# Kernel tuning notes

Hardware: AMD Instinct MI355X
Metric: run time of the kernel (lower is better)

The kernel has to match this reference:

```python
import jax, jax.numpy as jnp
import numpy as np

D_MODEL = 768
N_HEADS = 12
D_HEAD = D_MODEL // N_HEADS
B, T = 2, 4096


def setup_inputs() -> dict:
    key = jax.random.key(0)
    ks = jax.random.split(key, 9)
    s = 1.0 / np.sqrt(D_MODEL)
    x = jax.random.normal(ks[0], (B, T, D_MODEL), dtype=jnp.float32)
    Wq = jax.random.uniform(ks[1], (D_MODEL, D_MODEL), jnp.float32, -s, s)
    Wk = jax.random.uniform(ks[2], (D_MODEL, D_MODEL), jnp.float32, -s, s)
    Wv = jax.random.uniform(ks[3], (D_MODEL, D_MODEL), jnp.float32, -s, s)
    Wo = jax.random.uniform(ks[4], (D_MODEL, D_MODEL), jnp.float32, -s, s)
    bq = jax.random.uniform(ks[5], (D_MODEL,), jnp.float32, -s, s)
    bk = jax.random.uniform(ks[6], (D_MODEL,), jnp.float32, -s, s)
    bv = jax.random.uniform(ks[7], (D_MODEL,), jnp.float32, -s, s)
    bo = jax.random.uniform(ks[8], (D_MODEL,), jnp.float32, -s, s)
    return {"x": x, "Wq": Wq, "bq": bq, "Wk": Wk, "bk": bk,
            "Wv": Wv, "bv": bv, "Wo": Wo, "bo": bo}


def _split_heads(t):
    # [B, T, D] -> [B, H, T, d_head]
    Bc, Tc, _ = t.shape
    return t.reshape(Bc, Tc, N_HEADS, D_HEAD).transpose(0, 2, 1, 3)


def reference(x, Wq, bq, Wk, bk, Wv, bv, Wo, bo):
    scale = D_HEAD ** -0.5
    Q = _split_heads(x @ Wq.T + bq)
    K = _split_heads(x @ Wk.T + bk)
    V = _split_heads(x @ Wv.T + bv)
    scores = jnp.einsum('bhqd,bhkd->bhqk', Q, K) * scale  # [B,H,T,T]
    attn = jax.nn.softmax(scores, axis=-1)
    out = jnp.einsum('bhqk,bhkd->bhqd', attn, V)  # [B,H,T,d_head]
    out = out.transpose(0, 2, 1, 3).reshape(x.shape[0], x.shape[1], D_MODEL)
    return out @ Wo.T + bo
```

## Files before the change

kernel.cpp:

```cpp
#include <hip/hip_runtime.h>
#include <hip/hip_bf16.h>

#define DM 768
#define NH 12
#define TB 2
#define TT 4096
#define MM (TB*TT)
#define NQKV (3*DM)
#define NW (DM*DM)
#define NX (MM*DM)
#define CEQ 0.18033688f

typedef unsigned short u16;
typedef short s16x8 __attribute__((ext_vector_type(8)));
typedef unsigned short u16x8 __attribute__((ext_vector_type(8)));
typedef float f32x4 __attribute__((ext_vector_type(4)));
typedef float f32x16 __attribute__((ext_vector_type(16)));
typedef unsigned u32x4 __attribute__((ext_vector_type(4)));

#if __has_builtin(__builtin_amdgcn_exp2f)
#define EXP2 __builtin_amdgcn_exp2f
#else
#define EXP2 exp2f
#endif

__device__ __forceinline__ u16 f2bf(float f) {
  unsigned u = __builtin_bit_cast(unsigned, f);
  unsigned r = (u + 0x7FFFu + ((u >> 16) & 1u)) >> 16;
  return (u16)r;
}

__device__ __forceinline__ unsigned cvtpk(float lo, float hi) {
  unsigned r;
  asm("v_cvt_pk_bf16_f32 %0, %1, %2" : "=v"(r) : "v"(lo), "v"(hi));
  return r;
}

__device__ __forceinline__ void gload16(const void* g, void* l) {
  __builtin_amdgcn_global_load_lds(
      (const __attribute__((address_space(1))) void*)g,
      (__attribute__((address_space(3))) void*)l, 16, 0, 0);
}

__device__ __forceinline__ void plswap(unsigned a, unsigned b, unsigned& r0, unsigned& r1) {
#if __has_builtin(__builtin_amdgcn_permlane32_swap)
  auto rr = __builtin_amdgcn_permlane32_swap(a, b, false, false);
  unsigned tmp[2];
  __builtin_memcpy(tmp, &rr, 8);
  r0 = tmp[0]; r1 = tmp[1];
#else
  int hi_ = (threadIdx.x >> 5) & 1;
  unsigned bx = (unsigned)__shfl_xor((int)b, 32, 64);
  unsigned ax = (unsigned)__shfl_xor((int)a, 32, 64);
  r0 = hi_ ? bx : a;
  r1 = hi_ ? b : ax;
#endif
}

__device__ __forceinline__ float xhalf_sum(float v) {
  unsigned a = __builtin_bit_cast(unsigned, v), r0, r1;
  plswap(a, a, r0, r1);
  return __builtin_bit_cast(float, r0) + __builtin_bit_cast(float, r1);
}

__device__ __forceinline__ void repack2(const f32x16& sv, s16x8& fa, s16x8& fb) {
  {
    unsigned cA0 = cvtpk(sv[0], sv[1]),  cA1 = cvtpk(sv[2], sv[3]);
    unsigned cB0 = cvtpk(sv[4], sv[5]),  cB1 = cvtpk(sv[6], sv[7]);
    unsigned w0, w1, w2, w3;
    plswap(cA0, cB0, w0, w2);
    plswap(cA1, cB1, w1, w3);
    u32x4 w = {w0, w1, w2, w3};
    fa = __builtin_bit_cast(s16x8, w);
  }
  {
    unsigned cA0 = cvtpk(sv[8], sv[9]),   cA1 = cvtpk(sv[10], sv[11]);
    unsigned cB0 = cvtpk(sv[12], sv[13]), cB1 = cvtpk(sv[14], sv[15]);
    unsigned w0, w1, w2, w3;
    plswap(cA0, cB0, w0, w2);
    plswap(cA1, cB1, w1, w3);
    u32x4 w = {w0, w1, w2, w3};
    fb = __builtin_bit_cast(s16x8, w);
  }
}

__device__ __forceinline__ float tree16(const f32x16& u) {
  float a0 = u[0] + u[8],  a1 = u[1] + u[9],  a2 = u[2] + u[10], a3 = u[3] + u[11];
  float a4 = u[4] + u[12], a5 = u[5] + u[13], a6 = u[6] + u[14], a7 = u[7] + u[15];
  a0 += a4; a1 += a5; a2 += a6; a3 += a7;
  a0 += a2; a1 += a3;
  return a0 + a1;
}

__global__ __launch_bounds__(256) void cast_prep(
    const float* __restrict__ x, const float* __restrict__ wq,
    const float* __restrict__ wk, const float* __restrict__ wv,
    const float* __restrict__ wo, const float* __restrict__ bq,
    const float* __restrict__ bk, const float* __restrict__ bv,
    u16* __restrict__ xb, u16* __restrict__ wqkvb, u16* __restrict__ wob,
    float* __restrict__ bqkv) {
  int g = blockIdx.x * 256 + threadIdx.x;
  int e = g * 4;
  const float* src;
  u16* dst;
  if (e < NX) { src = x + e; dst = xb + e; }
  else {
    int e2 = e - NX;
    if (e2 < 3*NW) {
      const float* w = (e2 < NW) ? wq : (e2 < 2*NW ? wk : wv);
      int base = (e2 < NW) ? 0 : (e2 < 2*NW ? NW : 2*NW);
      src = w + (e2 - base); dst = wqkvb + e2;
    } else { int e3 = e2 - 3*NW; src = wo + e3; dst = wob + e3; }
  }
  float4 v = *(const float4*)src;
  ushort4 p;
  p.x = f2bf(v.x); p.y = f2bf(v.y); p.z = f2bf(v.z); p.w = f2bf(v.w);
  *(ushort4*)dst = p;
  if (blockIdx.x == 0) {
    for (int i = threadIdx.x; i < NQKV; i += 256)
      bqkv[i] = (i < DM) ? bq[i] : (i < 2*DM ? bk[i-DM] : bv[i-2*DM]);
  }
}

__global__ __launch_bounds__(256, 3) void gemm_qkv(
    const u16* __restrict__ A, const u16* __restrict__ W,
    const float* __restrict__ bias,
    u16* __restrict__ qb, u16* __restrict__ kb, u16* __restrict__ vt) {
  __shared__ __align__(16) u16 As[2][128*32], Bs[2][128*32];
  const int tid = threadIdx.x, lane = tid & 63, wave = tid >> 6;
  const int rg = lane & 15, cg = lane >> 4;
  int lin = blockIdx.y * 18 + blockIdx.x;
  int swz = (lin & 7) * 144 + (lin >> 3);
  const int m0 = (swz / 18) * 128, n0 = (swz % 18) * 128;
  const int wm = (wave >> 1) * 64, wn = (wave & 1) * 64;
  f32x4 acc[4][4];
#pragma unroll
  for (int i = 0; i < 4; i++)
#pragma unroll
    for (int j = 0; j < 4; j++) acc[i][j] = (f32x4){0.f,0.f,0.f,0.f};

  const u16* ga = A + (size_t)(m0 + (tid >> 2)) * DM + (tid & 3) * 8;
  const u16* gb = W + (size_t)(n0 + (tid >> 2)) * DM + (tid & 3) * 8;
  auto stage = [&](int kt, int buf) {
    int ko = kt * 32;
    char* la = (char*)&As[buf][0] + wave * 1024;
    char* lb = (char*)&Bs[buf][0] + wave * 1024;
    gload16(ga + ko,                    la);
    gload16(ga + (size_t)64*DM + ko,    la + 4096);
    gload16(gb + ko,                    lb);
    gload16(gb + (size_t)64*DM + ko,    lb + 4096);
  };

  stage(0, 0);
  __syncthreads();
  const int NT = DM / 32;
  int cur = 0;
  for (int kt = 0; kt < NT; ++kt) {
    if (kt + 1 < NT) stage(kt + 1, cur ^ 1);
    s16x8 af[4], bfv[4];
#pragma unroll
    for (int i = 0; i < 4; i++) af[i]  = *(const s16x8*)&As[cur][(wm + i*16 + rg)*32 + cg*8];
#pragma unroll
    for (int i = 0; i < 4; i++) bfv[i] = *(const s16x8*)&Bs[cur][(wn + i*16 + rg)*32 + cg*8];
    __builtin_amdgcn_s_setprio(1);
#pragma unroll
    for (int mi = 0; mi < 4; mi++)
#pragma unroll
      for (int ni = 0; ni < 4; ni++)
        acc[mi][ni] = __builtin_amdgcn_mfma_f32_16x16x32_bf16(af[mi], bfv[ni], acc[mi][ni], 0, 0, 0);
    __builtin_amdgcn_s_setprio(0);
    __syncthreads();
    cur ^= 1;
  }

#pragma unroll
  for (int ni = 0; ni < 4; ni++) {
    int o = n0 + wn + ni*16 + rg;
    float bia = bias[o];
    int mat = o / DM, d = o % DM;
    int head = d >> 6, dh = d & 63;
    if (mat == 2) {
#pragma unroll
      for (int mi = 0; mi < 4; mi++) {
        int m = m0 + wm + mi*16 + cg*4;
        int b = m >> 12, t = m & 4095;
        ushort4 pv;
        pv.x = f2bf(acc[mi][ni][0] + bia);
        pv.y = f2bf(acc[mi][ni][1] + bia);
        pv.z = f2bf(acc[mi][ni][2] + bia);
        pv.w = f2bf(acc[mi][ni][3] + bia);
        *(ushort4*)&vt[((size_t)((b*NH + head)*64 + dh))*TT + t] = pv;
      }
    } else {
      u16* outp = mat ? kb : qb;
      float sc = mat ? 1.0f : CEQ;
#pragma unroll
      for (int mi = 0; mi < 4; mi++) {
#pragma unroll
        for (int r = 0; r < 4; r++) {
          int m = m0 + wm + mi*16 + cg*4 + r;
          int b = m >> 12, t = m & 4095;
          outp[((size_t)((b*NH + head)*TT + t))*64 + dh] = f2bf((acc[mi][ni][r] + bia) * sc);
        }
      }
    }
  }
}

__global__ __launch_bounds__(128, 2) void attn5(
    const u16* __restrict__ qg, const u16* __restrict__ kg,
    const u16* __restrict__ vtg, u16* __restrict__ h) {
  __shared__ __align__(16) char smem[32768];
  const int tid = threadIdx.x, lane = tid & 63, wave = tid >> 6;
  const int ql = lane & 31, hi = lane >> 5;
  int lin = blockIdx.y * 32 + blockIdx.x;
  int swz = (lin & 7) * 96 + (lin >> 3);
  int qt = swz & 31, bh = swz >> 5;
  const int b = bh / NH, head = bh % NH;
  const size_t hb = (size_t)bh * TT * 64;

  const int qrowA = qt * 128 + wave * 64 + ql;
  const u16* qpA = qg + hb + (size_t)qrowA * 64 + hi * 8;
  s16x8 qfA[4], qfB[4];
#pragma unroll
  for (int ds = 0; ds < 4; ++ds) {
    qfA[ds] = *(const s16x8*)(qpA + ds * 16);
    qfB[ds] = *(const s16x8*)(qpA + 32*64 + ds * 16);
  }

  const int lr = lane >> 3;
  const int lc = ((lane & 7) ^ lr) * 16;
  const char* kSrc = (const char*)(kg + hb) + lr * 128 + lc;
  const char* vSrc = (const char*)(vtg + hb) + (size_t)lr * 8192 + lc;
  auto stage = [&](int kt, int buf) {
    char* lk = smem + buf * 16384 + wave * 4096;
    char* lv = lk + 8192;
    const char* gk = kSrc + (size_t)kt * 8192 + wave * 4096;
    const char* gv = vSrc + (size_t)kt * 128 + (size_t)wave * 262144;
#pragma unroll
    for (int i = 0; i < 4; ++i) {
      gload16(gk + i*1024,  lk + i*1024);
      gload16(gv + i*65536, lv + i*1024);
    }
  };

  f32x16 oA0 = {}, oA1 = {}, oB0 = {}, oB1 = {};
  float LA = 0.f, LB = 0.f;
  const int swb = (ql & 7) << 4;

  stage(0, 0);
  __syncthreads();

  const int NKT = TT / 64;
  int cur = 0;
  for (int kt = 0; kt < NKT; ++kt) {
    if (kt + 1 < NKT) stage(kt + 1, cur ^ 1);
    const char* Kt = smem + cur * 16384;
    const char* Vt = Kt + 8192;
#pragma unroll
    for (int c = 0; c < 2; ++c) {
      const char* bkc = Kt + (c*32 + ql) * 128;
      s16x8 kf[4];
#pragma unroll
      for (int ds = 0; ds < 4; ++ds)
        kf[ds] = *(const s16x8*)(bkc + ((ds*32 + hi*16) ^ swb));
      f32x16 sA = {}, sB = {};
      __builtin_amdgcn_s_setprio(1);
#pragma unroll
      for (int ds = 0; ds < 4; ++ds) {
        sA = __builtin_amdgcn_mfma_f32_32x32x16_bf16(kf[ds], qfA[ds], sA, 0, 0, 0);
        sB = __builtin_amdgcn_mfma_f32_32x32x16_bf16(kf[ds], qfB[ds], sB, 0, 0, 0);
      }
      __builtin_amdgcn_s_setprio(0);
      const char* bvc = Vt + ql * 128;
      s16x8 vf[2][2];
#pragma unroll
      for (int hh = 0; hh < 2; ++hh)
#pragma unroll
        for (int kc = 0; kc < 2; ++kc)
          vf[hh][kc] = *(const s16x8*)(bvc + hh*4096 + ((c*64 + kc*32 + hi*16) ^ swb));
#pragma unroll
      for (int i = 0; i < 16; ++i) sA[i] = EXP2(sA[i]);
#pragma unroll
      for (int i = 0; i < 16; ++i) sB[i] = EXP2(sB[i]);
      LA += tree16(sA);
      LB += tree16(sB);
      s16x8 pfA[2], pfB[2];
      repack2(sA, pfA[0], pfA[1]);
      repack2(sB, pfB[0], pfB[1]);
      __builtin_amdgcn_s_setprio(1);
#pragma unroll
      for (int kc = 0; kc < 2; ++kc) {
        oA0 = __builtin_amdgcn_mfma_f32_32x32x16_bf16(vf[0][kc], pfA[kc], oA0, 0, 0, 0);
        oB0 = __builtin_amdgcn_mfma_f32_32x32x16_bf16(vf[0][kc], pfB[kc], oB0, 0, 0, 0);
        oA1 = __builtin_amdgcn_mfma_f32_32x32x16_bf16(vf[1][kc], pfA[kc], oA1, 0, 0, 0);
        oB1 = __builtin_amdgcn_mfma_f32_32x32x16_bf16(vf[1][kc], pfB[kc], oB1, 0, 0, 0);
      }
      __builtin_amdgcn_s_setprio(0);
    }
    __syncthreads();
    cur ^= 1;
  }

  float invA = 1.f / xhalf_sum(LA);
  float invB = 1.f / xhalf_sum(LB);
  u16 (*ot)[72] = (u16(*)[72])smem;
#pragma unroll
  for (int db = 0; db < 2; ++db) {
    const f32x16& ovA = db ? oA1 : oA0;
    const f32x16& ovB = db ? oB1 : oB0;
#pragma unroll
    for (int i = 0; i < 8; ++i) {
      int d = db*32 + ((2*i) & 3) + 8*((2*i) >> 2) + 4*hi;
      *(unsigned*)&ot[wave*64 + ql][d]      = cvtpk(ovA[2*i]*invA, ovA[2*i+1]*invA);
      *(unsigned*)&ot[wave*64 + 32 + ql][d] = cvtpk(ovB[2*i]*invB, ovB[2*i+1]*invB);
    }
  }
  __syncthreads();
  const int row = wave*64 + lane;
  const u16* rowp = ot[row];
  const int qrow = qt*128 + row;
  u16* dst = h + (size_t)(b*TT + qrow) * DM + head*64;
#pragma unroll
  for (int i = 0; i < 4; ++i)
    *(u32x4*)(dst + i*16) = *(const u32x4*)(rowp + i*16);
#pragma unroll
  for (int i = 0; i < 4; ++i)
    *(u32x4*)(dst + i*16 + 8) = *(const u32x4*)(rowp + i*16 + 8);
}

__global__ __launch_bounds__(256, 3) void gemm_proj(
    const u16* __restrict__ A, const u16* __restrict__ W,
    const float* __restrict__ bias, float* __restrict__ out) {
  __shared__ __align__(16) u16 As[2][128*32], Bs[2][128*32];
  const int tid = threadIdx.x, lane = tid & 63, wave = tid >> 6;
  const int rg = lane & 15, cg = lane >> 4;
  int lin = blockIdx.y * 6 + blockIdx.x;
  int swz = (lin & 7) * 48 + (lin >> 3);
  const int m0 = (swz / 6) * 128, n0 = (swz % 6) * 128;
  const int wm = (wave >> 1) * 64, wn = (wave & 1) * 64;
  f32x4 acc[4][4];
#pragma unroll
  for (int i = 0; i < 4; i++)
#pragma unroll
    for (int j = 0; j < 4; j++) acc[i][j] = (f32x4){0.f,0.f,0.f,0.f};

  const u16* ga = A + (size_t)(m0 + (tid >> 2)) * DM + (tid & 3) * 8;
  const u16* gb = W + (size_t)(n0 + (tid >> 2)) * DM + (tid & 3) * 8;
  auto stage = [&](int kt, int buf) {
    int ko = kt * 32;
    char* la = (char*)&As[buf][0] + wave * 1024;
    char* lb = (char*)&Bs[buf][0] + wave * 1024;
    gload16(ga + ko,                    la);
    gload16(ga + (size_t)64*DM + ko,    la + 4096);
    gload16(gb + ko,                    lb);
    gload16(gb + (size_t)64*DM + ko,    lb + 4096);
  };

  stage(0, 0);
  __syncthreads();
  const int NT = DM / 32;
  int cur = 0;
  for (int kt = 0; kt < NT; ++kt) {
    if (kt + 1 < NT) stage(kt + 1, cur ^ 1);
    s16x8 af[4], bfv[4];
#pragma unroll
    for (int i = 0; i < 4; i++) af[i]  = *(const s16x8*)&As[cur][(wm + i*16 + rg)*32 + cg*8];
#pragma unroll
    for (int i = 0; i < 4; i++) bfv[i] = *(const s16x8*)&Bs[cur][(wn + i*16 + rg)*32 + cg*8];
    __builtin_amdgcn_s_setprio(1);
#pragma unroll
    for (int mi = 0; mi < 4; mi++)
#pragma unroll
      for (int ni = 0; ni < 4; ni++)
        acc[mi][ni] = __builtin_amdgcn_mfma_f32_16x16x32_bf16(af[mi], bfv[ni], acc[mi][ni], 0, 0, 0);
    __builtin_amdgcn_s_setprio(0);
    __syncthreads();
    cur ^= 1;
  }
#pragma unroll
  for (int ni = 0; ni < 4; ni++) {
    int o = n0 + wn + ni*16 + rg;
    float bia = bias[o];
#pragma unroll
    for (int mi = 0; mi < 4; mi++) {
#pragma unroll
      for (int r = 0; r < 4; r++) {
        int m = m0 + wm + mi*16 + cg*4 + r;
        out[(size_t)m * DM + o] = acc[mi][ni][r] + bia;
      }
    }
  }
}

extern "C" void kernel_launch(void* const* d_in, const int* in_sizes, int n_in,
                              void* d_out, int out_size, void* d_ws, size_t ws_size,
                              hipStream_t stream) {
  (void)in_sizes; (void)n_in; (void)out_size; (void)ws_size;
  const float* x  = (const float*)d_in[0];
  const float* Wq = (const float*)d_in[1];
  const float* bq = (const float*)d_in[2];
  const float* Wk = (const float*)d_in[3];
  const float* bk = (const float*)d_in[4];
  const float* Wv = (const float*)d_in[5];
  const float* bv = (const float*)d_in[6];
  const float* Wo = (const float*)d_in[7];
  const float* bo = (const float*)d_in[8];
  float* out = (float*)d_out;

  char* ws = (char*)d_ws;
  size_t off = 0;
  auto alloc = [&](size_t bytes) {
    char* p = ws + off;
    off = (off + bytes + 255) & ~(size_t)255;
    return p;
  };
  u16*   xb    = (u16*)alloc((size_t)NX * 2);
  u16*   wqkvb = (u16*)alloc((size_t)3 * NW * 2);
  u16*   wob   = (u16*)alloc((size_t)NW * 2);
  float* bqkv  = (float*)alloc((size_t)NQKV * 4);
  u16*   qb    = (u16*)alloc((size_t)NX * 2);
  u16*   kb    = (u16*)alloc((size_t)NX * 2);
  u16*   vtb   = (u16*)alloc((size_t)NX * 2);
  u16*   hbuf  = xb;

  cast_prep<<<(NX + 4*NW) / 4 / 256, 256, 0, stream>>>(x, Wq, Wk, Wv, Wo, bq, bk, bv,
                                                       xb, wqkvb, wob, bqkv);
  gemm_qkv<<<dim3(18, 64), 256, 0, stream>>>(xb, wqkvb, bqkv, qb, kb, vtb);
  attn5<<<dim3(32, TB*NH), 128, 0, stream>>>(qb, kb, vtb, hbuf);
  gemm_proj<<<dim3(6, 64), 256, 0, stream>>>(hbuf, wob, bo, out);
}
```

Baseline: 207.0 us.

## Split attention key tiles across wave pairs with shared-memory reduction

```diff
diff --git a/kernel.cpp b/kernel.cpp
--- a/kernel.cpp
+++ b/kernel.cpp
@@ -90,6 +90,21 @@
   a0 += a4; a1 += a5; a2 += a6; a3 += a7;
   a0 += a2; a1 += a3;
   return a0 + a1;
+}
+
+__device__ __forceinline__ void dump16(float* p, const f32x16& ov) {
+#pragma unroll
+  for (int c4 = 0; c4 < 4; ++c4) {
+    f32x4 t = {ov[c4*4], ov[c4*4+1], ov[c4*4+2], ov[c4*4+3]};
+    *(f32x4*)(p + c4*256) = t;
+  }
+}
+__device__ __forceinline__ void add16(const float* p, f32x16& ov) {
+#pragma unroll
+  for (int c4 = 0; c4 < 4; ++c4) {
+    f32x4 t = *(const f32x4*)(p + c4*256);
+    ov[c4*4] += t[0]; ov[c4*4+1] += t[1]; ov[c4*4+2] += t[2]; ov[c4*4+3] += t[3];
+  }
 }
 
 __global__ __launch_bounds__(256) void cast_prep(
@@ -207,19 +222,20 @@
   }
 }
 
-__global__ __launch_bounds__(128, 2) void attn5(
+__global__ __launch_bounds__(256, 3) void attn6(
     const u16* __restrict__ qg, const u16* __restrict__ kg,
     const u16* __restrict__ vtg, u16* __restrict__ h) {
-  __shared__ __align__(16) char smem[32768];
+  __shared__ __align__(16) char smem[33792];
   const int tid = threadIdx.x, lane = tid & 63, wave = tid >> 6;
   const int ql = lane & 31, hi = lane >> 5;
+  const int wq = wave & 1, wk = wave >> 1;
   int lin = blockIdx.y * 32 + blockIdx.x;
   int swz = (lin & 7) * 96 + (lin >> 3);
   int qt = swz & 31, bh = swz >> 5;
   const int b = bh / NH, head = bh % NH;
   const size_t hb = (size_t)bh * TT * 64;
 
-  const int qrowA = qt * 128 + wave * 64 + ql;
+  const int qrowA = qt * 128 + wq * 64 + ql;
   const u16* qpA = qg + hb + (size_t)qrowA * 64 + hi * 8;
   s16x8 qfA[4], qfB[4];
 #pragma unroll
@@ -232,16 +248,16 @@
   const int lc = ((lane & 7) ^ lr) * 16;
   const char* kSrc = (const char*)(kg + hb) + lr * 128 + lc;
   const char* vSrc = (const char*)(vtg + hb) + (size_t)lr * 8192 + lc;
+  char* ldsK = smem + wave * 2048;
   auto stage = [&](int kt, int buf) {
-    char* lk = smem + buf * 16384 + wave * 4096;
+    char* lk = ldsK + buf * 16384;
     char* lv = lk + 8192;
-    const char* gk = kSrc + (size_t)kt * 8192 + wave * 4096;
-    const char* gv = vSrc + (size_t)kt * 128 + (size_t)wave * 262144;
-#pragma unroll
-    for (int i = 0; i < 4; ++i) {
-      gload16(gk + i*1024,  lk + i*1024);
-      gload16(gv + i*65536, lv + i*1024);
-    }
+    const char* gk = kSrc + (size_t)kt * 8192 + wave * 2048;
+    const char* gv = vSrc + (size_t)kt * 128 + (size_t)wave * 131072;
+    gload16(gk,          lk);
+    gload16(gk + 1024,   lk + 1024);
+    gload16(gv,          lv);
+    gload16(gv + 65536,  lv + 1024);
   };
 
   f32x16 oA0 = {}, oA1 = {}, oB0 = {}, oB1 = {};
@@ -257,76 +273,100 @@
     if (kt + 1 < NKT) stage(kt + 1, cur ^ 1);
     const char* Kt = smem + cur * 16384;
     const char* Vt = Kt + 8192;
-#pragma unroll
-    for (int c = 0; c < 2; ++c) {
-      const char* bkc = Kt + (c*32 + ql) * 128;
-      s16x8 kf[4];
-#pragma unroll
-      for (int ds = 0; ds < 4; ++ds)
-        kf[ds] = *(const s16x8*)(bkc + ((ds*32 + hi*16) ^ swb));
-      f32x16 sA = {}, sB = {};
-      __builtin_amdgcn_s_setprio(1);
-#pragma unroll
-      for (int ds = 0; ds < 4; ++ds) {
-        sA = __builtin_amdgcn_mfma_f32_32x32x16_bf16(kf[ds], qfA[ds], sA, 0, 0, 0);
-        sB = __builtin_amdgcn_mfma_f32_32x32x16_bf16(kf[ds], qfB[ds], sB, 0, 0, 0);
-      }
-      __builtin_amdgcn_s_setprio(0);
-      const char* bvc = Vt + ql * 128;
-      s16x8 vf[2][2];
-#pragma unroll
-      for (int hh = 0; hh < 2; ++hh)
-#pragma unroll
-        for (int kc = 0; kc < 2; ++kc)
-          vf[hh][kc] = *(const s16x8*)(bvc + hh*4096 + ((c*64 + kc*32 + hi*16) ^ swb));
-#pragma unroll
-      for (int i = 0; i < 16; ++i) sA[i] = EXP2(sA[i]);
-#pragma unroll
-      for (int i = 0; i < 16; ++i) sB[i] = EXP2(sB[i]);
-      LA += tree16(sA);
-      LB += tree16(sB);
-      s16x8 pfA[2], pfB[2];
-      repack2(sA, pfA[0], pfA[1]);
-      repack2(sB, pfB[0], pfB[1]);
-      __builtin_amdgcn_s_setprio(1);
-#pragma unroll
-      for (int kc = 0; kc < 2; ++kc) {
-        oA0 = __builtin_amdgcn_mfma_f32_32x32x16_bf16(vf[0][kc], pfA[kc], oA0, 0, 0, 0);
-        oB0 = __builtin_amdgcn_mfma_f32_32x32x16_bf16(vf[0][kc], pfB[kc], oB0, 0, 0, 0);
-        oA1 = __builtin_amdgcn_mfma_f32_32x32x16_bf16(vf[1][kc], pfA[kc], oA1, 0, 0, 0);
-        oB1 = __builtin_amdgcn_mfma_f32_32x32x16_bf16(vf[1][kc], pfB[kc], oB1, 0, 0, 0);
-      }
-      __builtin_amdgcn_s_setprio(0);
+
+    const char* bkc = Kt + (wk*32 + ql) * 128;
+    s16x8 kf[4];
+#pragma unroll
+    for (int ds = 0; ds < 4; ++ds)
+      kf[ds] = *(const s16x8*)(bkc + ((ds*32 + hi*16) ^ swb));
+    f32x16 sA = {}, sB = {};
+    __builtin_amdgcn_s_setprio(1);
+#pragma unroll
+    for (int ds = 0; ds < 4; ++ds) {
+      sA = __builtin_amdgcn_mfma_f32_32x32x16_bf16(kf[ds], qfA[ds], sA, 0, 0, 0);
+      sB = __builtin_amdgcn_mfma_f32_32x32x16_bf16(kf[ds], qfB[ds], sB, 0, 0, 0);
     }
+    __builtin_amdgcn_s_setprio(0);
+
+    const char* bvc = Vt + ql * 128;
+    s16x8 vf[2][2];
+#pragma unroll
+    for (int hh = 0; hh < 2; ++hh)
+#pragma unroll
+      for (int kc = 0; kc < 2; ++kc)
+        vf[hh][kc] = *(const s16x8*)(bvc + hh*4096 + ((wk*64 + kc*32 + hi*16) ^ swb));
+
+#pragma unroll
+    for (int i = 0; i < 16; ++i) sA[i] = EXP2(sA[i]);
+#pragma unroll
+    for (int i = 0; i < 16; ++i) sB[i] = EXP2(sB[i]);
+    LA += tree16(sA);
+    LB += tree16(sB);
+
+    s16x8 pfA[2], pfB[2];
+    repack2(sA, pfA[0], pfA[1]);
+    repack2(sB, pfB[0], pfB[1]);
+
+    __builtin_amdgcn_s_setprio(1);
+#pragma unroll
+    for (int kc = 0; kc < 2; ++kc) {
+      oA0 = __builtin_amdgcn_mfma_f32_32x32x16_bf16(vf[0][kc], pfA[kc], oA0, 0, 0, 0);
+      oB0 = __builtin_amdgcn_mfma_f32_32x32x16_bf16(vf[0][kc], pfB[kc], oB0, 0, 0, 0);
+      oA1 = __builtin_amdgcn_mfma_f32_32x32x16_bf16(vf[1][kc], pfA[kc], oA1, 0, 0, 0);
+      oB1 = __builtin_amdgcn_mfma_f32_32x32x16_bf16(vf[1][kc], pfB[kc], oB1, 0, 0, 0);
+    }
+    __builtin_amdgcn_s_setprio(0);
+
     __syncthreads();
     cur ^= 1;
   }
 
-  float invA = 1.f / xhalf_sum(LA);
-  float invB = 1.f / xhalf_sum(LB);
+  float* po = (float*)smem;
+  float* pl = (float*)(smem + 32768);
+  if (wk) {
+    float* pb = po + wq*4096 + lane*4;
+    dump16(pb,        oA0);
+    dump16(pb + 1024, oA1);
+    dump16(pb + 2048, oB0);
+    dump16(pb + 3072, oB1);
+    pl[wq*128 + lane]      = LA;
+    pl[wq*128 + 64 + lane] = LB;
+  }
+  __syncthreads();
+  if (!wk) {
+    const float* pb = po + wq*4096 + lane*4;
+    add16(pb,        oA0);
+    add16(pb + 1024, oA1);
+    add16(pb + 2048, oB0);
+    add16(pb + 3072, oB1);
+    LA += pl[wq*128 + lane];
+    LB += pl[wq*128 + 64 + lane];
+  }
+  __syncthreads();
+
   u16 (*ot)[72] = (u16(*)[72])smem;
-#pragma unroll
-  for (int db = 0; db < 2; ++db) {
-    const f32x16& ovA = db ? oA1 : oA0;
-    const f32x16& ovB = db ? oB1 : oB0;
-#pragma unroll
-    for (int i = 0; i < 8; ++i) {
-      int d = db*32 + ((2*i) & 3) + 8*((2*i) >> 2) + 4*hi;
-      *(unsigned*)&ot[wave*64 + ql][d]      = cvtpk(ovA[2*i]*invA, ovA[2*i+1]*invA);
-      *(unsigned*)&ot[wave*64 + 32 + ql][d] = cvtpk(ovB[2*i]*invB, ovB[2*i+1]*invB);
+  if (!wk) {
+    float invA = 1.f / xhalf_sum(LA);
+    float invB = 1.f / xhalf_sum(LB);
+#pragma unroll
+    for (int db = 0; db < 2; ++db) {
+      const f32x16& ovA = db ? oA1 : oA0;
+      const f32x16& ovB = db ? oB1 : oB0;
+#pragma unroll
+      for (int i = 0; i < 8; ++i) {
+        int d = db*32 + ((2*i) & 3) + 8*((2*i) >> 2) + 4*hi;
+        *(unsigned*)&ot[wq*64 + ql][d]      = cvtpk(ovA[2*i]*invA, ovA[2*i+1]*invA);
+        *(unsigned*)&ot[wq*64 + 32 + ql][d] = cvtpk(ovB[2*i]*invB, ovB[2*i+1]*invB);
+      }
     }
   }
   __syncthreads();
-  const int row = wave*64 + lane;
-  const u16* rowp = ot[row];
-  const int qrow = qt*128 + row;
-  u16* dst = h + (size_t)(b*TT + qrow) * DM + head*64;
+  const int row = tid >> 1, half = tid & 1;
+  const u16* rowp = &ot[row][half*32];
+  u16* dst = h + (size_t)(b*TT + qt*128 + row) * DM + head*64 + half*32;
 #pragma unroll
   for (int i = 0; i < 4; ++i)
-    *(u32x4*)(dst + i*16) = *(const u32x4*)(rowp + i*16);
-#pragma unroll
-  for (int i = 0; i < 4; ++i)
-    *(u32x4*)(dst + i*16 + 8) = *(const u32x4*)(rowp + i*16 + 8);
+    *(u32x4*)(dst + i*8) = *(const u32x4*)(rowp + i*8);
 }
 
 __global__ __launch_bounds__(256, 3) void gemm_proj(
@@ -427,6 +467,6 @@
   cast_prep<<<(NX + 4*NW) / 4 / 256, 256, 0, stream>>>(x, Wq, Wk, Wv, Wo, bq, bk, bv,
                                                        xb, wqkvb, wob, bqkv);
   gemm_qkv<<<dim3(18, 64), 256, 0, stream>>>(xb, wqkvb, bqkv, qb, kb, vtb);
-  attn5<<<dim3(32, TB*NH), 128, 0, stream>>>(qb, kb, vtb, hbuf);
+  attn6<<<dim3(32, TB*NH), 256, 0, stream>>>(qb, kb, vtb, hbuf);
   gemm_proj<<<dim3(6, 64), 256, 0, stream>>>(hbuf, wob, bo, out);
 }
```

New measurement: 262.9 us. 1.27x slower.
